# Kernel tuning notes

Hardware: AMD Instinct MI355X
Metric: run time of the kernel (lower is better)

The kernel has to match this reference:

```python
import jax, jax.numpy as jnp
import numpy as np

N = 1048576
HID = 256
GEO = 15
POS_LAT = 3 + 10 * 2 * 3  # 63
DIR_LAT = 3 + 4 * 2 * 3   # 27
AABB_MIN = -1.5
AABB_MAX = 1.5


def sinus_enc(x, min_deg, max_deg):
    # x: [..., 3] -> [..., 3 + (max_deg-min_deg)*2*3] (identity + sin/cos bands)
    scales = 2.0 ** jnp.arange(min_deg, max_deg, dtype=x.dtype)
    xb = (x[..., None, :] * scales[:, None]).reshape(
        x.shape[:-1] + ((max_deg - min_deg) * x.shape[-1],))
    latent = jnp.sin(jnp.concatenate([xb, xb + 0.5 * np.pi], axis=-1))
    return jnp.concatenate([x, latent], axis=-1)


def trunc_exp(x):
    return jnp.exp(x)


def setup_inputs() -> dict:
    key = jax.random.key(0)
    ks = jax.random.split(key, 12)
    positions = jax.random.uniform(ks[0], (N, 3), dtype=jnp.float32,
                                   minval=AABB_MIN, maxval=AABB_MAX)
    directions = jax.random.normal(ks[1], (N, 3), dtype=jnp.float32)
    s = 0.05
    return {
        "positions": positions,
        "directions": directions,
        "W1": jax.random.normal(ks[2], (POS_LAT, HID), jnp.float32) * s,
        "b1": jnp.zeros((HID,), jnp.float32),
        "W2": jax.random.normal(ks[3], (HID, HID), jnp.float32) * s,
        "b2": jnp.zeros((HID,), jnp.float32),
        "W3": jax.random.normal(ks[4], (HID, HID), jnp.float32) * s,
        "b3": jnp.zeros((HID,), jnp.float32),
        "W4": jax.random.normal(ks[5], (HID, 1 + GEO), jnp.float32) * s,
        "b4": jnp.zeros((1 + GEO,), jnp.float32),
        "Wc1": jax.random.normal(ks[6], (GEO + DIR_LAT, HID // 2), jnp.float32) * s,
        "bc1": jnp.zeros((HID // 2,), jnp.float32),
        "Wc2": jax.random.normal(ks[7], (HID // 2, 3), jnp.float32) * s,
        "bc2": jnp.zeros((3,), jnp.float32),
    }


def reference(positions, directions, W1, b1, W2, b2, W3, b3, W4, b4,
              Wc1, bc1, Wc2, bc2):
    # normalize positions into [-1, 1] within the aabb
    x = (positions - AABB_MIN) / (AABB_MAX - AABB_MIN) * 2.0 - 1.0
    pe = sinus_enc(x, 0, 10)  # [N, 63]
    h = jax.nn.relu(pe @ W1 + b1)
    h = jax.nn.relu(h @ W2 + b2)
    h = jax.nn.relu(h @ W3 + b3)
    h = h @ W4 + b4  # [N, 16]
    density = trunc_exp(h[..., 0:1] - 1.0)  # [N, 1]
    feat = h[..., 1:]  # [N, 15]

    nrm = jnp.linalg.norm(directions, axis=-1, keepdims=True)
    d = directions / jnp.maximum(nrm, 1e-12)
    de = sinus_enc(d, 0, 4)  # [N, 27]
    hc = jnp.concatenate([feat, de], axis=-1)  # [N, 42]
    hc = jax.nn.relu(hc @ Wc1 + bc1)
    rgb = jax.nn.sigmoid(hc @ Wc2 + bc2)  # [N, 3]
    return rgb, density
```

## Files before the change

### kernel.cpp

```cpp
#include <hip/hip_runtime.h>

typedef unsigned short u16;
typedef __attribute__((ext_vector_type(8))) short short8;
typedef __attribute__((ext_vector_type(4))) float f32x4;
typedef __attribute__((ext_vector_type(16))) float f32x16;
typedef __attribute__((ext_vector_type(2))) unsigned int u32x2;

#define NPTS 1048576
#define TILES 128
#define NBLK (NPTS / (32 * TILES))
#define HPE 72
#define HPB 264
#define HPF 136

__device__ __forceinline__ u16 f2b(float f) {
    return (u16)((__float_as_uint(f) + 0x8000u) >> 16);
}
#define INV2PI 0.15915494309189535f
__device__ __forceinline__ float sinrev(float t) {
    t = t - floorf(t);
    return __builtin_amdgcn_sinf(t);
}

__global__ void prep_weights(const float* __restrict__ W1, const float* __restrict__ b1,
                             const float* __restrict__ W2,
                             const float* __restrict__ W3, const float* __restrict__ W4,
                             const float* __restrict__ Wc1, const float* __restrict__ bc1,
                             const float* __restrict__ Wc2,
                             u16* __restrict__ ws) {
    int i = blockIdx.x * 256 + threadIdx.x;
    if (i < 16384) { int n = i >> 6, k = i & 63;  ws[i]          = (k < 63) ? f2b(W1[k * 256 + n]) : f2b(b1[n]); return; }
    i -= 16384;
    if (i < 65536) { int n = i >> 8, k = i & 255; ws[16384 + i]  = f2b(W2[k * 256 + n]); return; }
    i -= 65536;
    if (i < 65536) { int n = i >> 8, k = i & 255; ws[81920 + i]  = f2b(W3[k * 256 + n]); return; }
    i -= 65536;
    if (i < 4096)  { int n = i >> 8, k = i & 255; ws[147456 + i] = f2b(W4[k * 16 + n]); return; }
    i -= 4096;
    if (i < 8192)  { int n = i >> 6, k = i & 63;
                     ws[151552 + i] = (k < 42) ? f2b(Wc1[k * 128 + n]) : ((k == 42) ? f2b(bc1[n]) : (u16)0); return; }
    i -= 8192;
    if (i < 2048)  { int n = i >> 7, k = i & 127; ws[159744 + i] = (n < 3) ? f2b(Wc2[k * 3 + n]) : (u16)0; return; }
}

template <bool BIAS>
__device__ __forceinline__ void epi32(const f32x16& acc, u16* rowp, const float* bias,
                                      int nbase, int kh) {
#pragma unroll
    for (int g = 0; g < 4; ++g) {
        const int mq = nbase + 8 * g + 4 * kh;
        float v[4];
#pragma unroll
        for (int j = 0; j < 4; ++j) v[j] = acc[4 * g + j];
        if (BIAS) {
            const f32x4 bi = *(const f32x4*)(bias + mq);
#pragma unroll
            for (int j = 0; j < 4; ++j) v[j] += bi[j];
        }
#pragma unroll
        for (int j = 0; j < 4; ++j) v[j] = fmaxf(v[j], 0.f);
        unsigned int u[4];
#pragma unroll
        for (int j = 0; j < 4; ++j) u[j] = __float_as_uint(v[j]) + 0x8000u;
        u32x2 d;
        d.x = __builtin_amdgcn_perm(u[1], u[0], 0x07060302);
        d.y = __builtin_amdgcn_perm(u[3], u[2], 0x07060302);
        *(u32x2*)(rowp + mq) = d;
    }
}

template <int NKT, bool BIAS>
__device__ __forceinline__ void layer32(const short8* wr, const u16* src, int ss,
                                        u16* dst, int ds, const float* bias,
                                        int nbase, int ln, int kh) {
    f32x16 acc;
#pragma unroll
    for (int r = 0; r < 16; ++r) acc[r] = 0.f;
#pragma unroll
    for (int kt = 0; kt < NKT; ++kt) {
        const short8 bA = *(const short8*)(src + ln * ss + kt * 16 + kh * 8);
        acc = __builtin_amdgcn_mfma_f32_32x32x16_bf16(wr[kt], bA, acc, 0, 0, 0);
    }
    epi32<BIAS>(acc, dst + ln * ds, bias, nbase, kh);
}

__global__ __launch_bounds__(1024, 4) void ngp_fused(
    const float* __restrict__ pos, const float* __restrict__ dir, const u16* __restrict__ ws,
    const float* __restrict__ b2, const float* __restrict__ b3,
    const float* __restrict__ b4, const float* __restrict__ bc2,
    float* __restrict__ out) {
    __shared__ __align__(16) u16 sE[32][HPE];
    __shared__ __align__(16) u16 sB[32][HPB];
    __shared__ __align__(16) u16 sC[32][HPB];
    __shared__ __align__(16) u16 sD[32][HPB];
    __shared__ __align__(16) u16 sG[2][32][HPE];
    __shared__ __align__(16) u16 sF[32][HPF];
    const int t = threadIdx.x;
    const int lane = t & 63;
    const int w = t >> 6;
    const int bw = w - 8;
    const int ln = lane & 31, kh = lane >> 5;
    const int lr = lane & 15, q = lane >> 4;

    const u16* WT1  = ws;
    const u16* WT2  = ws + 16384;
    const u16* WT3  = ws + 81920;
    const u16* WT4  = ws + 147456;
    const u16* WTc1 = ws + 151552;
    const u16* WTc2 = ws + 159744;

    short8 wrA[16], wrB[4];
    {
        const u16* pA = (w < 8) ? WT2 + (size_t)(w * 32 + ln) * 256 + kh * 8
                                : WT3 + (size_t)(bw * 32 + ln) * 256 + kh * 8;
#pragma unroll
        for (int kt = 0; kt < 16; ++kt) wrA[kt] = *(const short8*)(pA + kt * 16);
        const u16* pB = (w < 8)  ? WT1 + (size_t)(w * 32 + ln) * 64 + kh * 8
                      : (bw < 4) ? WTc1 + (size_t)(bw * 32 + ln) * 64 + kh * 8
                                 : WT1 + (size_t)ln * 64 + kh * 8;
#pragma unroll
        for (int kt = 0; kt < 4; ++kt) wrB[kt] = *(const short8*)(pB + kt * 16);
    }

    for (int i = 0; i <= TILES + 1; ++i) {
        const bool doE = (i < TILES);
        const bool doM = (i >= 1 && i <= TILES);
        const bool doH = (i >= 2);
        const long rbE = ((long)blockIdx.x * TILES + i) * 32;
        const long rbM = rbE - 32;
        const long rbH = rbE - 64;
        u16* sGe = &sG[i & 1][0][0];
        u16* sGf = &sG[(i + 1) & 1][0][0];

        if (doE && t < 512) {
            if (t < 256) {
                const int r = t >> 3, g = t & 7;
                const long row = rbE + r;
                float xn[3];
#pragma unroll
                for (int c = 0; c < 3; ++c) xn[c] = pos[row * 3 + c] * (1.0f / 1.5f);
                if (g < 5) {
#pragma unroll
                    for (int dd = 0; dd < 2; ++dd) {
                        const int d = 2 * g + dd;
                        const float sc = (float)(1 << d);
#pragma unroll
                        for (int c = 0; c < 3; ++c) {
                            float tv = xn[c] * sc * INV2PI;
                            sE[r][3 + d * 3 + c]  = f2b(sinrev(tv));
                            sE[r][33 + d * 3 + c] = f2b(sinrev(tv + 0.25f));
                        }
                    }
                } else if (g == 5) {
                    sE[r][0] = f2b(xn[0]); sE[r][1] = f2b(xn[1]); sE[r][2] = f2b(xn[2]);
                    sE[r][63] = 0x3F80;
                }
            } else {
                const int t2 = t - 256;
                const int r = t2 >> 3, g = t2 & 7;
                const long row = rbE + r;
                u16* gr = sGe + r * HPE;
                const float dx = dir[row * 3 + 0];
                const float dy = dir[row * 3 + 1];
                const float dz = dir[row * 3 + 2];
                if (g < 6) {
                    const float nrm = sqrtf(dx * dx + dy * dy + dz * dz);
                    const float inv = 1.f / fmaxf(nrm, 1e-12f);
                    const float dn[3] = {dx * inv, dy * inv, dz * inv};
                    if (g < 4) {
                        const float sc = (float)(1 << g);
#pragma unroll
                        for (int c = 0; c < 3; ++c) {
                            float tv = dn[c] * sc * INV2PI;
                            gr[18 + g * 3 + c] = f2b(sinrev(tv));
                            gr[30 + g * 3 + c] = f2b(sinrev(tv + 0.25f));
                        }
                    } else if (g == 4) {
                        gr[15] = f2b(dn[0]); gr[16] = f2b(dn[1]); gr[17] = f2b(dn[2]);
                    } else {
                        gr[42] = 0x3F80;
#pragma unroll
                        for (int c = 43; c < 50; ++c) gr[c] = 0;
                    }
                } else if (g == 6) {
#pragma unroll
                    for (int c = 50; c < 57; ++c) gr[c] = 0;
                } else {
#pragma unroll
                    for (int c = 57; c < 64; ++c) gr[c] = 0;
                }
            }
        }
        if (doM && w >= 8)
            layer32<16, true>(wrA, &sC[0][0], HPB, &sD[0][0], HPB, b3, bw * 32, ln, kh);
        __syncthreads();

        if (doE && w < 8)
            layer32<4, false>(wrB, &sE[0][0], HPE, &sB[0][0], HPB, nullptr, w * 32, ln, kh);
        if (doM && w >= 8 && (bw == 4 || bw == 5)) {
            const int rbase = (bw - 4) * 16;
            f32x4 acc = {0.f, 0.f, 0.f, 0.f};
#pragma unroll
            for (int kt = 0; kt < 8; ++kt) {
                const short8 aF = *(const short8*)&sD[rbase + lr][kt * 32 + q * 8];
                const short8 bF = *(const short8*)(WT4 + lr * 256 + kt * 32 + q * 8);
                acc = __builtin_amdgcn_mfma_f32_16x16x32_bf16(aF, bF, acc, 0, 0, 0);
            }
            const float bi = b4[lr];
#pragma unroll
            for (int r = 0; r < 4; ++r) {
                const float v = acc[r] + bi;
                const int gm = rbase + q * 4 + r;
                if (lr == 0)
                    out[3 * (long)NPTS + rbM + gm] = __expf(v - 1.f);
                else
                    sGf[gm * HPE + lr - 1] = f2b(v);
            }
        }
        if (doH && w >= 8 && (bw == 6 || bw == 7)) {
            const int rbase = (bw - 6) * 16;
            f32x4 acc = {0.f, 0.f, 0.f, 0.f};
#pragma unroll
            for (int kt = 0; kt < 4; ++kt) {
                const short8 aF = *(const short8*)&sF[rbase + lr][kt * 32 + q * 8];
                const short8 bF = *(const short8*)(WTc2 + lr * 128 + kt * 32 + q * 8);
                acc = __builtin_amdgcn_mfma_f32_16x16x32_bf16(aF, bF, acc, 0, 0, 0);
            }
            if (lr < 3) {
                const float bi = bc2[lr];
#pragma unroll
                for (int r = 0; r < 4; ++r) {
                    const float v = acc[r] + bi;
                    const float sg = 1.f / (1.f + __expf(-v));
                    out[(rbH + rbase + q * 4 + r) * 3 + lr] = sg;
                }
            }
        }
        __syncthreads();

        if (doE && w < 8)
            layer32<16, true>(wrA, &sB[0][0], HPB, &sC[0][0], HPB, b2, w * 32, ln, kh);
        if (doM && w >= 8 && bw < 4)
            layer32<4, false>(wrB, sGf, HPE, &sF[0][0], HPF, nullptr, bw * 32, ln, kh);
        __syncthreads();
    }
}

extern "C" void kernel_launch(void* const* d_in, const int* in_sizes, int n_in,
                              void* d_out, int out_size, void* d_ws, size_t ws_size,
                              hipStream_t stream) {
    const float* pos = (const float*)d_in[0];
    const float* dir = (const float*)d_in[1];
    const float* W1  = (const float*)d_in[2];
    const float* b1  = (const float*)d_in[3];
    const float* W2  = (const float*)d_in[4];
    const float* b2  = (const float*)d_in[5];
    const float* W3  = (const float*)d_in[6];
    const float* b3  = (const float*)d_in[7];
    const float* W4  = (const float*)d_in[8];
    const float* b4  = (const float*)d_in[9];
    const float* Wc1 = (const float*)d_in[10];
    const float* bc1 = (const float*)d_in[11];
    const float* Wc2 = (const float*)d_in[12];
    const float* bc2 = (const float*)d_in[13];
    u16* ws   = (u16*)d_ws;
    float* out = (float*)d_out;

    prep_weights<<<633, 256, 0, stream>>>(W1, b1, W2, W3, W4, Wc1, bc1, Wc2, ws);
    ngp_fused<<<NBLK, 1024, 0, stream>>>(pos, dir, ws, b2, b3, b4, bc2, out);
}
```

Before: 636.0 us.

## Pipeline encoding with prefetch and merge stages to cut barriers per tile

```diff
diff --git a/kernel.cpp b/kernel.cpp
--- a/kernel.cpp
+++ b/kernel.cpp
@@ -84,17 +84,86 @@
     epi32<BIAS>(acc, dst + ln * ds, bias, nbase, kh);
 }
 
+__device__ __forceinline__ void enc_preload(const float* __restrict__ pos,
+                                            const float* __restrict__ dir,
+                                            long rb, int t, float* v) {
+    if (t < 256) {
+        const long row = rb + (t >> 3);
+        v[0] = pos[row * 3 + 0]; v[1] = pos[row * 3 + 1]; v[2] = pos[row * 3 + 2];
+    } else {
+        const long row = rb + ((t - 256) >> 3);
+        v[0] = dir[row * 3 + 0]; v[1] = dir[row * 3 + 1]; v[2] = dir[row * 3 + 2];
+    }
+}
+
+__device__ __forceinline__ void enc_compute(const float* v, int t, u16* sEj, u16* sGj) {
+    if (t < 256) {
+        const int r = t >> 3, g = t & 7;
+        float xn[3];
+#pragma unroll
+        for (int c = 0; c < 3; ++c) xn[c] = v[c] * (1.0f / 1.5f);
+        u16* er = sEj + r * HPE;
+        if (g < 5) {
+#pragma unroll
+            for (int dd = 0; dd < 2; ++dd) {
+                const int d = 2 * g + dd;
+                const float sc = (float)(1 << d);
+#pragma unroll
+                for (int c = 0; c < 3; ++c) {
+                    float tv = xn[c] * sc * INV2PI;
+                    er[3 + d * 3 + c]  = f2b(sinrev(tv));
+                    er[33 + d * 3 + c] = f2b(sinrev(tv + 0.25f));
+                }
+            }
+        } else if (g == 5) {
+            er[0] = f2b(xn[0]); er[1] = f2b(xn[1]); er[2] = f2b(xn[2]);
+            er[63] = 0x3F80;
+        }
+    } else {
+        const int t2 = t - 256;
+        const int r = t2 >> 3, g = t2 & 7;
+        u16* gr = sGj + r * HPE;
+        const float dx = v[0], dy = v[1], dz = v[2];
+        if (g < 6) {
+            const float nrm = sqrtf(dx * dx + dy * dy + dz * dz);
+            const float inv = 1.f / fmaxf(nrm, 1e-12f);
+            const float dn[3] = {dx * inv, dy * inv, dz * inv};
+            if (g < 4) {
+                const float sc = (float)(1 << g);
+#pragma unroll
+                for (int c = 0; c < 3; ++c) {
+                    float tv = dn[c] * sc * INV2PI;
+                    gr[18 + g * 3 + c] = f2b(sinrev(tv));
+                    gr[30 + g * 3 + c] = f2b(sinrev(tv + 0.25f));
+                }
+            } else if (g == 4) {
+                gr[15] = f2b(dn[0]); gr[16] = f2b(dn[1]); gr[17] = f2b(dn[2]);
+            } else {
+                gr[42] = 0x3F80;
+#pragma unroll
+                for (int c = 43; c < 50; ++c) gr[c] = 0;
+            }
+        } else if (g == 6) {
+#pragma unroll
+            for (int c = 50; c < 57; ++c) gr[c] = 0;
+        } else {
+#pragma unroll
+            for (int c = 57; c < 64; ++c) gr[c] = 0;
+        }
+    }
+}
+
 __global__ __launch_bounds__(1024, 4) void ngp_fused(
     const float* __restrict__ pos, const float* __restrict__ dir, const u16* __restrict__ ws,
     const float* __restrict__ b2, const float* __restrict__ b3,
     const float* __restrict__ b4, const float* __restrict__ bc2,
     float* __restrict__ out) {
-    __shared__ __align__(16) u16 sE[32][HPE];
+    __shared__ __align__(16) u16 sE[2][32][HPE];
     __shared__ __align__(16) u16 sB[32][HPB];
     __shared__ __align__(16) u16 sC[32][HPB];
     __shared__ __align__(16) u16 sD[32][HPB];
-    __shared__ __align__(16) u16 sG[2][32][HPE];
-    __shared__ __align__(16) u16 sF[32][HPF];
+    __shared__ __align__(16) u16 sG[4][32][HPE];
+    __shared__ __align__(16) u16 sF[2][32][HPF];
     const int t = threadIdx.x;
     const int lane = t & 63;
     const int w = t >> 6;
@@ -122,82 +191,38 @@
         for (int kt = 0; kt < 4; ++kt) wrB[kt] = *(const short8*)(pB + kt * 16);
     }
 
-    for (int i = 0; i <= TILES + 1; ++i) {
-        const bool doE = (i < TILES);
-        const bool doM = (i >= 1 && i <= TILES);
-        const bool doH = (i >= 2);
-        const long rbE = ((long)blockIdx.x * TILES + i) * 32;
-        const long rbM = rbE - 32;
-        const long rbH = rbE - 64;
-        u16* sGe = &sG[i & 1][0][0];
-        u16* sGf = &sG[(i + 1) & 1][0][0];
-
-        if (doE && t < 512) {
-            if (t < 256) {
-                const int r = t >> 3, g = t & 7;
-                const long row = rbE + r;
-                float xn[3];
-#pragma unroll
-                for (int c = 0; c < 3; ++c) xn[c] = pos[row * 3 + c] * (1.0f / 1.5f);
-                if (g < 5) {
-#pragma unroll
-                    for (int dd = 0; dd < 2; ++dd) {
-                        const int d = 2 * g + dd;
-                        const float sc = (float)(1 << d);
-#pragma unroll
-                        for (int c = 0; c < 3; ++c) {
-                            float tv = xn[c] * sc * INV2PI;
-                            sE[r][3 + d * 3 + c]  = f2b(sinrev(tv));
-                            sE[r][33 + d * 3 + c] = f2b(sinrev(tv + 0.25f));
-                        }
-                    }
-                } else if (g == 5) {
-                    sE[r][0] = f2b(xn[0]); sE[r][1] = f2b(xn[1]); sE[r][2] = f2b(xn[2]);
-                    sE[r][63] = 0x3F80;
-                }
-            } else {
-                const int t2 = t - 256;
-                const int r = t2 >> 3, g = t2 & 7;
-                const long row = rbE + r;
-                u16* gr = sGe + r * HPE;
-                const float dx = dir[row * 3 + 0];
-                const float dy = dir[row * 3 + 1];
-                const float dz = dir[row * 3 + 2];
-                if (g < 6) {
-                    const float nrm = sqrtf(dx * dx + dy * dy + dz * dz);
-                    const float inv = 1.f / fmaxf(nrm, 1e-12f);
-                    const float dn[3] = {dx * inv, dy * inv, dz * inv};
-                    if (g < 4) {
-                        const float sc = (float)(1 << g);
-#pragma unroll
-                        for (int c = 0; c < 3; ++c) {
-                            float tv = dn[c] * sc * INV2PI;
-                            gr[18 + g * 3 + c] = f2b(sinrev(tv));
-                            gr[30 + g * 3 + c] = f2b(sinrev(tv + 0.25f));
-                        }
-                    } else if (g == 4) {
-                        gr[15] = f2b(dn[0]); gr[16] = f2b(dn[1]); gr[17] = f2b(dn[2]);
-                    } else {
-                        gr[42] = 0x3F80;
-#pragma unroll
-                        for (int c = 43; c < 50; ++c) gr[c] = 0;
-                    }
-                } else if (g == 6) {
-#pragma unroll
-                    for (int c = 50; c < 57; ++c) gr[c] = 0;
-                } else {
-#pragma unroll
-                    for (int c = 57; c < 64; ++c) gr[c] = 0;
-                }
-            }
-        }
-        if (doM && w >= 8)
+    {
+        float pv[3];
+        if (t < 512) {
+            enc_preload(pos, dir, (long)blockIdx.x * TILES * 32, t, pv);
+            enc_compute(pv, t, &sE[0][0][0], &sG[0][0][0]);
+        }
+        __syncthreads();
+    }
+
+    for (int i = 0; i <= TILES + 2; ++i) {
+        const bool dL1  = (i < TILES);
+        const bool dEnc = (i + 1 < TILES);
+        const bool dL3  = (i >= 1 && i <= TILES);
+        const bool dC1  = (i >= 2 && i <= TILES + 1);
+        const bool dHd  = (i >= 3);
+
+        float pv[3];
+        if (dEnc && t < 512)
+            enc_preload(pos, dir, ((long)blockIdx.x * TILES + i + 1) * 32, t, pv);
+        if (dL1 && w < 8)
+            layer32<4, false>(wrB, &sE[i & 1][0][0], HPE, &sB[0][0], HPB, nullptr, w * 32, ln, kh);
+        if (dL3 && w >= 8)
             layer32<16, true>(wrA, &sC[0][0], HPB, &sD[0][0], HPB, b3, bw * 32, ln, kh);
+        if (dEnc && t < 512)
+            enc_compute(pv, t, &sE[(i + 1) & 1][0][0], &sG[(i + 1) & 3][0][0]);
         __syncthreads();
 
-        if (doE && w < 8)
-            layer32<4, false>(wrB, &sE[0][0], HPE, &sB[0][0], HPB, nullptr, w * 32, ln, kh);
-        if (doM && w >= 8 && (bw == 4 || bw == 5)) {
+        if (dL1 && w < 8)
+            layer32<16, true>(wrA, &sB[0][0], HPB, &sC[0][0], HPB, b2, w * 32, ln, kh);
+        if (dL3 && w >= 8 && (bw == 4 || bw == 5)) {
+            const long rbM = ((long)blockIdx.x * TILES + i - 1) * 32;
+            u16* sGf = &sG[(i - 1) & 3][0][0];
             const int rbase = (bw - 4) * 16;
             f32x4 acc = {0.f, 0.f, 0.f, 0.f};
 #pragma unroll
@@ -217,12 +242,16 @@
                     sGf[gm * HPE + lr - 1] = f2b(v);
             }
         }
-        if (doH && w >= 8 && (bw == 6 || bw == 7)) {
+        if (dC1 && w >= 8 && bw < 4)
+            layer32<4, false>(wrB, &sG[(i - 2) & 3][0][0], HPE, &sF[(i - 2) & 1][0][0], HPF,
+                              nullptr, bw * 32, ln, kh);
+        if (dHd && w >= 8 && (bw == 6 || bw == 7)) {
+            const long rbH = ((long)blockIdx.x * TILES + i - 3) * 32;
             const int rbase = (bw - 6) * 16;
             f32x4 acc = {0.f, 0.f, 0.f, 0.f};
 #pragma unroll
             for (int kt = 0; kt < 4; ++kt) {
-                const short8 aF = *(const short8*)&sF[rbase + lr][kt * 32 + q * 8];
+                const short8 aF = *(const short8*)&sF[(i - 3) & 1][rbase + lr][kt * 32 + q * 8];
                 const short8 bF = *(const short8*)(WTc2 + lr * 128 + kt * 32 + q * 8);
                 acc = __builtin_amdgcn_mfma_f32_16x16x32_bf16(aF, bF, acc, 0, 0, 0);
             }
@@ -236,12 +265,6 @@
                 }
             }
         }
-        __syncthreads();
-
-        if (doE && w < 8)
-            layer32<16, true>(wrA, &sB[0][0], HPB, &sC[0][0], HPB, b2, w * 32, ln, kh);
-        if (doM && w >= 8 && bw < 4)
-            layer32<4, false>(wrB, sGf, HPE, &sF[0][0], HPF, nullptr, bw * 32, ln, kh);
         __syncthreads();
     }
 }
```

Result: faster. 562.4 us (-11.6%).
